# Optimization experiments

Hardware: AMD Instinct MI355X
Metric: run time of the kernel (lower is better)

## Reference

```python
import jax, jax.numpy as jnp
import numpy as np

B, S, H, NH = 32, 512, 768, 12
EC, EU = 4, 4
CAP = 1.0
DH = H // NH
CAPACITY = int(CAP * B / EC)  # Switch-style capacity per common expert


def setup_inputs() -> dict:
    key = jax.random.key(0)
    ks = jax.random.split(key, 10)
    s = 0.02
    E = EC + EU  # experts stacked: [0:EC]=common, [EC:]=unique
    return {
        "hidden_states": jax.random.normal(ks[0], (B, S, H), jnp.float32),
        "attention_mask": jnp.zeros((B, S), jnp.float32),  # additive mask
        "Wq": jax.random.normal(ks[1], (E, H, H), jnp.float32) * s,
        "bq": jnp.zeros((E, H), jnp.float32),
        "Wk": jax.random.normal(ks[2], (E, H, H), jnp.float32) * s,
        "bk": jnp.zeros((E, H), jnp.float32),
        "Wv": jax.random.normal(ks[3], (E, H, H), jnp.float32) * s,
        "bv": jnp.zeros((E, H), jnp.float32),
        "Wo": jax.random.normal(ks[4], (E, H, H), jnp.float32) * s,
        "bo": jnp.zeros((E, H), jnp.float32),
        "Wsc": jax.random.normal(ks[5], (H, EC), jnp.float32) * s,
        "bsc": jnp.zeros((EC,), jnp.float32),
        "Wsu": jax.random.normal(ks[6], (H, EU), jnp.float32) * s,
        "bsu": jnp.zeros((EU,), jnp.float32),
    }


def reference(hidden_states, attention_mask, Wq, bq, Wk, bk, Wv, bv, Wo, bo,
              Wsc, bsc, Wsu, bsu):
    # ---- common routing (per-sequence top-1 over mean-pooled tokens) ----
    h_mean = hidden_states.mean(axis=1)                       # [B,H]
    pc = jax.nn.softmax(h_mean @ Wsc + bsc, axis=-1)          # [B,EC]
    rc = jnp.argmax(pc, axis=-1)                              # [B]
    pc_max = jnp.max(pc, axis=-1)                             # [B]
    # capacity drop: within each expert keep the CAPACITY highest-prob seqs
    order = jnp.argsort(-pc_max)                              # global desc sort
    oh = jax.nn.one_hot(rc[order], EC, dtype=jnp.int32)       # [B,EC]
    rank = jnp.take_along_axis(jnp.cumsum(oh, axis=0), rc[order][:, None], 1)[:, 0]
    kept = jnp.zeros((B,), bool).at[order].set(rank <= CAPACITY)

    # ---- unique routing for dropped sequences (mean is per-sequence, so
    #      computing on the full batch and masking matches torch) ----
    pu = jax.nn.softmax(h_mean @ Wsu + bsu, axis=-1)          # [B,EU]
    ru = jnp.argmax(pu, axis=-1)
    pu_max = jnp.max(pu, axis=-1)

    # per-sequence expert index into stacked [EC+EU] expert params
    eidx = jnp.where(kept, rc, EC + ru)                       # [B]
    # scaling factor p/stop_grad(p): ==1 in fwd, routes grads to the gate
    scale = jnp.where(kept,
                      pc_max / jax.lax.stop_gradient(pc_max),
                      pu_max / jax.lax.stop_gradient(pu_max))

    # ---- gather-dispatch: per-sequence expert weights ----
    Wq_b, Wk_b, Wv_b, Wo_b = Wq[eidx], Wk[eidx], Wv[eidx], Wo[eidx]  # [B,H,H]
    bq_b, bk_b, bv_b, bo_b = bq[eidx], bk[eidx], bv[eidx], bo[eidx]  # [B,H]

    def heads(t):  # [B,S,H] -> [B,NH,S,DH]
        return t.reshape(B, S, NH, DH).transpose(0, 2, 1, 3)

    q = heads(jnp.einsum('bsh,bhd->bsd', hidden_states, Wq_b) + bq_b[:, None, :])
    k = heads(jnp.einsum('bsh,bhd->bsd', hidden_states, Wk_b) + bk_b[:, None, :])
    v = heads(jnp.einsum('bsh,bhd->bsd', hidden_states, Wv_b) + bv_b[:, None, :])

    scores = jnp.einsum('bhsd,bhtd->bhst', q, k) / np.float32(np.sqrt(DH))
    scores = scores + attention_mask[:, None, None, :]        # additive mask
    attn = jax.nn.softmax(scores, axis=-1)
    ctx = jnp.einsum('bhst,bhtd->bhsd', attn, v)
    ctx = ctx.transpose(0, 2, 1, 3).reshape(B, S, H)

    out = jnp.einsum('bsh,bhd->bsd', ctx, Wo_b) + bo_b[:, None, :]
    return out * scale[:, None, None]
```

## Files before the change

kernel.cpp:

```cpp
#include <hip/hip_runtime.h>
#include <hip/hip_bf16.h>

#define B_ 32
#define S_ 512
#define H_ 768
#define NH_ 12
#define DH_ 64
#define EC_ 4
#define CAPN_ 8

using short8  = __attribute__((ext_vector_type(8))) short;
using floatx4 = __attribute__((ext_vector_type(4))) float;
using bf16 = __hip_bfloat16;

__device__ __forceinline__ void gl_lds16(const void* g, void* l) {
  __builtin_amdgcn_global_load_lds(
      (const __attribute__((address_space(1))) unsigned int*)g,
      (__attribute__((address_space(3))) unsigned int*)l, 16, 0, 0);
}

__global__ void k_mean_convert(const float* __restrict__ X, bf16* __restrict__ Xh,
                               float* __restrict__ partial) {
  int idx = blockIdx.x * 256 + threadIdx.x;
  int b = idx / H_, h = idx - b * H_;
  int s0 = blockIdx.y * 64;
  size_t base = ((size_t)b * S_ + s0) * H_ + h;
  float sum = 0.f;
#pragma unroll 8
  for (int s = 0; s < 64; ++s) {
    float v = X[base + (size_t)s * H_];
    Xh[base + (size_t)s * H_] = __float2bfloat16(v);
    sum += v;
  }
  partial[(size_t)blockIdx.y * (B_ * H_) + idx] = sum;
}

__global__ void k_mean_reduce(const float* __restrict__ partial, float* __restrict__ hmean) {
  int idx = blockIdx.x * 256 + threadIdx.x;
  float s = 0.f;
#pragma unroll
  for (int c = 0; c < 8; ++c) s += partial[(size_t)c * (B_ * H_) + idx];
  hmean[idx] = s * (1.f / 512.f);
}

__global__ void k_wt(const float* __restrict__ Wq, const float* __restrict__ Wk,
                     const float* __restrict__ Wv, const float* __restrict__ Wo,
                     bf16* __restrict__ Wt) {
  __shared__ float tile[32][33];
  int z = blockIdx.z;
  const float* Wbase = (z < 8 ? Wq : z < 16 ? Wk : z < 24 ? Wv : Wo) + (size_t)(z & 7) * H_ * H_;
  int k0 = blockIdx.x * 32, n0 = blockIdx.y * 32;
  int tj = threadIdx.x & 31, ti = threadIdx.x >> 5;
#pragma unroll
  for (int r = 0; r < 4; ++r)
    tile[ti + r * 8][tj] = Wbase[(size_t)(k0 + ti + r * 8) * H_ + n0 + tj];
  __syncthreads();
  bf16* out = Wt + (size_t)z * H_ * H_;
#pragma unroll
  for (int r = 0; r < 4; ++r)
    out[(size_t)(n0 + ti + r * 8) * H_ + k0 + tj] = __float2bfloat16(tile[tj][ti + r * 8]);
}

__global__ void k_route(const float* __restrict__ hmean,
                        const float* __restrict__ Wsc, const float* __restrict__ bsc,
                        const float* __restrict__ Wsu, const float* __restrict__ bsu,
                        int* __restrict__ eidx) {
  __shared__ float logit[B_][8];
  __shared__ float pcmax[B_];
  __shared__ int rc_s[B_], ru_s[B_];
  int t = threadIdx.x;
  {
    int b = t >> 3, g = t & 7;
    const float* w = (g < 4) ? (Wsc + g) : (Wsu + (g - 4));
    float acc = (g < 4) ? bsc[g] : bsu[g - 4];
    const float* hm = hmean + (size_t)b * H_;
    for (int hh = 0; hh < H_; ++hh) acc += hm[hh] * w[hh * 4];
    logit[b][g] = acc;
  }
  __syncthreads();
  if (t < B_) {
    float m = logit[t][0]; int a = 0;
    for (int e = 1; e < 4; ++e) if (logit[t][e] > m) { m = logit[t][e]; a = e; }
    float s = 0.f;
    for (int e = 0; e < 4; ++e) s += expf(logit[t][e] - m);
    pcmax[t] = 1.f / s;
    rc_s[t] = a;
    float mu = logit[t][4]; int au = 0;
    for (int e = 1; e < 4; ++e) if (logit[t][4 + e] > mu) { mu = logit[t][4 + e]; au = e; }
    ru_s[t] = au;
  }
  __syncthreads();
  if (t == 0) {
    bool used[B_], kept[B_];
    int cnt[EC_] = {0, 0, 0, 0};
    for (int i = 0; i < B_; ++i) used[i] = false;
    for (int i = 0; i < B_; ++i) {
      int best = 0; float bv = -1e30f;
      for (int j = 0; j < B_; ++j)
        if (!used[j] && pcmax[j] > bv) { bv = pcmax[j]; best = j; }
      used[best] = true;
      kept[best] = (++cnt[rc_s[best]] <= CAPN_);
    }
    for (int i = 0; i < B_; ++i)
      eidx[i] = kept[i] ? rc_s[i] : EC_ + ru_s[i];
  }
}

template <int OMODE>
__global__ __launch_bounds__(256) void k_gemm(
    const bf16* __restrict__ A, const bf16* __restrict__ Wt,
    const float* __restrict__ bias0, const float* __restrict__ bias1,
    const float* __restrict__ bias2,
    void* out0, void* out1, void* out2,
    const int* __restrict__ eidx, int mat0) {
  __shared__ __align__(16) char lds[32768];
  int bz = blockIdx.z;
  int b = blockIdx.y;
  int e = eidx[b];
  int mtile = blockIdx.x & 3, ntile = blockIdx.x >> 2;
  int m0 = mtile * 128, n0 = ntile * 128;
  const bf16* Ab = A + (size_t)b * S_ * H_;
  const bf16* Wb = Wt + (size_t)((mat0 + bz) * 8 + e) * H_ * H_;
  const float* bias = ((bz == 0) ? bias0 : (bz == 1) ? bias1 : bias2) + (size_t)e * H_;
  void* outp = (bz == 0) ? out0 : (bz == 1) ? out1 : out2;

  int t = threadIdx.x, lane = t & 63, w = t >> 6;
  int wm = (w & 1) * 64, wn = (w >> 1) * 64;
  int lm = lane & 15, lq = lane >> 4;

  floatx4 acc[4][4] = {};
  for (int kt = 0; kt < 12; ++kt) {
    __syncthreads();
#pragma unroll
    for (int r = 0; r < 8; ++r) {
      int c = t + r * 256;
      const bf16* g;
      if (c < 1024) {
        int mm = c >> 3, pos = c & 7, kc = pos ^ (mm & 7);
        g = Ab + (size_t)(m0 + mm) * H_ + kt * 64 + kc * 8;
      } else {
        int c2 = c - 1024;
        int nn = c2 >> 3, pos = c2 & 7, kc = pos ^ (nn & 7);
        g = Wb + (size_t)(n0 + nn) * H_ + kt * 64 + kc * 8;
      }
      gl_lds16(g, lds + (size_t)c * 16);
    }
    __syncthreads();
#pragma unroll
    for (int kf = 0; kf < 2; ++kf) {
      int kc = kf * 4 + lq;
      short8 af[4], bf[4];
#pragma unroll
      for (int mf = 0; mf < 4; ++mf) {
        int mm = wm + mf * 16 + lm;
        af[mf] = *(const short8*)(lds + ((size_t)(mm * 8 + (kc ^ (mm & 7)))) * 16);
      }
#pragma unroll
      for (int nf = 0; nf < 4; ++nf) {
        int nn = wn + nf * 16 + lm;
        bf[nf] = *(const short8*)(lds + 16384 + ((size_t)(nn * 8 + (kc ^ (nn & 7)))) * 16);
      }
#pragma unroll
      for (int mf = 0; mf < 4; ++mf)
#pragma unroll
        for (int nf = 0; nf < 4; ++nf)
          acc[mf][nf] = __builtin_amdgcn_mfma_f32_16x16x32_bf16(af[mf], bf[nf], acc[mf][nf], 0, 0, 0);
    }
  }
#pragma unroll
  for (int mf = 0; mf < 4; ++mf) {
#pragma unroll
    for (int nf = 0; nf < 4; ++nf) {
      int n = n0 + wn + nf * 16 + lm;
      float bv = bias[n];
      int mrow = m0 + wm + mf * 16 + lq * 4;
      size_t rowbase = ((size_t)b * S_ + mrow) * H_ + n;
#pragma unroll
      for (int r = 0; r < 4; ++r) {
        float v = acc[mf][nf][r] + bv;
        if (OMODE == 0) ((bf16*)outp)[rowbase + (size_t)r * H_] = __float2bfloat16(v);
        else            ((float*)outp)[rowbase + (size_t)r * H_] = v;
      }
    }
  }
}

__global__ void k_vt(const bf16* __restrict__ V, bf16* __restrict__ Vt) {
  __shared__ __align__(16) unsigned short tile[64][72];
  int sb = blockIdx.x, h = blockIdx.y, b = blockIdx.z;
  int t = threadIdx.x;
  const unsigned short* src =
      (const unsigned short*)V + ((size_t)(b * S_ + sb * 64)) * H_ + h * DH_;
#pragma unroll
  for (int r = 0; r < 2; ++r) {
    int i = (t >> 3) + r * 32, j8 = t & 7;
    uint4 val = *(const uint4*)(src + (size_t)i * H_ + j8 * 8);
    *(uint4*)&tile[i][j8 * 8] = val;
  }
  __syncthreads();
  unsigned short* dst =
      (unsigned short*)Vt + ((size_t)((b * NH_ + h) * 64 + sb * 8)) * 512;
#pragma unroll
  for (int r = 0; r < 2; ++r) {
    int c = t + r * 256;
    int scl = c >> 6, dh = c & 63;
    union { unsigned short u[8]; uint4 v4; } pk;
#pragma unroll
    for (int j = 0; j < 8; ++j) pk.u[j] = tile[scl * 8 + j][dh];
    *(uint4*)(dst + (size_t)c * 8) = pk.v4;
  }
}

__global__ __launch_bounds__(256) void k_attn(
    const bf16* __restrict__ Q, const bf16* __restrict__ K,
    const bf16* __restrict__ Vt, const float* __restrict__ mask,
    bf16* __restrict__ Ctx) {
  __shared__ __align__(16) char ldsQ[4096];
  __shared__ __align__(16) char ldsK[8192];
  __shared__ __align__(16) bf16 sc[32 * 520];
  __shared__ float inv_sum[32];

  int qt = blockIdx.x, h = blockIdx.y, b = blockIdx.z;
  int q0 = qt * 32;
  int t = threadIdx.x, lane = t & 63, w = t >> 6;
  int lm = lane & 15, lq = lane >> 4;

  {
    int s = t >> 3, pos = t & 7, kc = pos ^ (s & 7);
    const bf16* g = Q + ((size_t)(b * S_ + q0 + s)) * H_ + h * DH_ + kc * 8;
    gl_lds16(g, ldsQ + (size_t)t * 16);
  }
  __syncthreads();

  short8 qf[2][2];
#pragma unroll
  for (int mf = 0; mf < 2; ++mf)
#pragma unroll
    for (int kf = 0; kf < 2; ++kf) {
      int srow = mf * 16 + lm, kc = kf * 4 + lq;
      qf[mf][kf] = *(const short8*)(ldsQ + ((size_t)(srow * 8 + (kc ^ (srow & 7)))) * 16);
    }

  for (int kt = 0; kt < 8; ++kt) {
#pragma unroll
    for (int r = 0; r < 2; ++r) {
      int c = t + r * 256;
      int s = c >> 3, pos = c & 7, kc = pos ^ (s & 7);
      const bf16* g = K + ((size_t)(b * S_ + kt * 64 + s)) * H_ + h * DH_ + kc * 8;
      gl_lds16(g, ldsK + (size_t)c * 16);
    }
    __syncthreads();
    floatx4 a2[2] = {};
#pragma unroll
    for (int kf = 0; kf < 2; ++kf) {
      int row = w * 16 + lm, kc = kf * 4 + lq;
      short8 bfr = *(const short8*)(ldsK + ((size_t)(row * 8 + (kc ^ (row & 7)))) * 16);
#pragma unroll
      for (int mf = 0; mf < 2; ++mf)
        a2[mf] = __builtin_amdgcn_mfma_f32_16x16x32_bf16(qf[mf][kf], bfr, a2[mf], 0, 0, 0);
    }
    int col = kt * 64 + w * 16 + lm;
    float mv = mask[(size_t)b * S_ + col];
#pragma unroll
    for (int mf = 0; mf < 2; ++mf)
#pragma unroll
      for (int r = 0; r < 4; ++r) {
        int row = mf * 16 + lq * 4 + r;
        sc[row * 520 + col] = __float2bfloat16(a2[mf][r] * 0.125f + mv);
      }
    __syncthreads();
  }

  {
    int row = t >> 3, seg = t & 7;
    bf16* rp = sc + row * 520;
    float rm = -1e30f;
#pragma unroll 8
    for (int i = 0; i < 64; ++i) rm = fmaxf(rm, __bfloat162float(rp[seg + i * 8]));
    rm = fmaxf(rm, __shfl_xor(rm, 1));
    rm = fmaxf(rm, __shfl_xor(rm, 2));
    rm = fmaxf(rm, __shfl_xor(rm, 4));
    float sum = 0.f;
#pragma unroll 8
    for (int i = 0; i < 64; ++i) {
      float e = __expf(__bfloat162float(rp[seg + i * 8]) - rm);
      sum += e;
      rp[seg + i * 8] = __float2bfloat16(e);
    }
    sum += __shfl_xor(sum, 1);
    sum += __shfl_xor(sum, 2);
    sum += __shfl_xor(sum, 4);
    if (seg == 0) inv_sum[row] = 1.f / sum;
  }
  __syncthreads();

  floatx4 oacc[2] = {};
  const bf16* vbase = Vt + ((size_t)(b * NH_ + h)) * 64 * 512;
  for (int kt = 0; kt < 8; ++kt) {
#pragma unroll
    for (int r = 0; r < 2; ++r) {
      int c = t + r * 256;
      gl_lds16(vbase + ((size_t)(kt * 512 + c)) * 8, ldsK + (size_t)c * 16);
    }
    __syncthreads();
#pragma unroll
    for (int kf = 0; kf < 2; ++kf) {
      int dh = w * 16 + lm;
      short8 bfr = *(const short8*)(ldsK + ((size_t)((kf * 4 + lq) * 64 + dh)) * 16);
#pragma unroll
      for (int mf = 0; mf < 2; ++mf) {
        int row = mf * 16 + lm;
        short8 af = *(const short8*)((const char*)sc +
                        ((size_t)(row * 520 + kt * 64 + kf * 32 + lq * 8)) * 2);
        oacc[mf] = __builtin_amdgcn_mfma_f32_16x16x32_bf16(af, bfr, oacc[mf], 0, 0, 0);
      }
    }
    __syncthreads();
  }
  int dh = w * 16 + lm;
#pragma unroll
  for (int mf = 0; mf < 2; ++mf)
#pragma unroll
    for (int r = 0; r < 4; ++r) {
      int row = mf * 16 + lq * 4 + r;
      float v = oacc[mf][r] * inv_sum[row];
      Ctx[((size_t)(b * S_ + q0 + row)) * H_ + h * DH_ + dh] = __float2bfloat16(v);
    }
}

extern "C" void kernel_launch(void* const* d_in, const int* in_sizes, int n_in,
                              void* d_out, int out_size, void* d_ws, size_t ws_size,
                              hipStream_t stream) {
  const float* X    = (const float*)d_in[0];
  const float* mask = (const float*)d_in[1];
  const float* Wq   = (const float*)d_in[2];
  const float* bq   = (const float*)d_in[3];
  const float* Wk   = (const float*)d_in[4];
  const float* bk   = (const float*)d_in[5];
  const float* Wv   = (const float*)d_in[6];
  const float* bv   = (const float*)d_in[7];
  const float* Wo   = (const float*)d_in[8];
  const float* bo   = (const float*)d_in[9];
  const float* Wsc  = (const float*)d_in[10];
  const float* bsc  = (const float*)d_in[11];
  const float* Wsu  = (const float*)d_in[12];
  const float* bsu  = (const float*)d_in[13];

  char* ws = (char*)d_ws;
  int*   eidx    = (int*)ws;
  float* partial = (float*)(ws + 256);
  float* hmean   = (float*)(ws + 786688);
  bf16*  Xh      = (bf16*)(ws + 884992);
  bf16*  Wt      = (bf16*)(ws + 26050816);
  bf16*  qb      = (bf16*)(ws + 63799552);
  bf16*  kb      = (bf16*)(ws + 88965376);
  bf16*  vb      = (bf16*)(ws + 114131200);
  bf16*  Vt      = (bf16*)(ws + 139297024);
  bf16*  ctx     = Xh;

  k_mean_convert<<<dim3(96, 8), 256, 0, stream>>>(X, Xh, partial);
  k_mean_reduce<<<96, 256, 0, stream>>>(partial, hmean);
  k_wt<<<dim3(24, 24, 32), 256, 0, stream>>>(Wq, Wk, Wv, Wo, Wt);
  k_route<<<1, 256, 0, stream>>>(hmean, Wsc, bsc, Wsu, bsu, eidx);
  k_gemm<0><<<dim3(24, 32, 3), 256, 0, stream>>>(Xh, Wt, bq, bk, bv,
                                                 (void*)qb, (void*)kb, (void*)vb, eidx, 0);
  k_vt<<<dim3(8, NH_, B_), 256, 0, stream>>>(vb, Vt);
  k_attn<<<dim3(16, NH_, B_), 256, 0, stream>>>(qb, kb, Vt, mask, ctx);
  k_gemm<1><<<dim3(24, 32, 1), 256, 0, stream>>>(ctx, Wt, bo, bo, bo,
                                                 d_out, d_out, d_out, eidx, 3);
}
```

Measured before the change: 538.6 us.

## Fuse V transpose into QKV GEMM epilogue and register-resident softmax with double-buffered attention

```diff
diff --git a/kernel.cpp b/kernel.cpp
--- a/kernel.cpp
+++ b/kernel.cpp
@@ -178,135 +178,179 @@
 #pragma unroll
       for (int r = 0; r < 4; ++r) {
         float v = acc[mf][nf][r] + bv;
-        if (OMODE == 0) ((bf16*)outp)[rowbase + (size_t)r * H_] = __float2bfloat16(v);
-        else            ((float*)outp)[rowbase + (size_t)r * H_] = v;
-      }
-    }
-  }
-}
-
-__global__ void k_vt(const bf16* __restrict__ V, bf16* __restrict__ Vt) {
-  __shared__ __align__(16) unsigned short tile[64][72];
-  int sb = blockIdx.x, h = blockIdx.y, b = blockIdx.z;
-  int t = threadIdx.x;
-  const unsigned short* src =
-      (const unsigned short*)V + ((size_t)(b * S_ + sb * 64)) * H_ + h * DH_;
-#pragma unroll
-  for (int r = 0; r < 2; ++r) {
-    int i = (t >> 3) + r * 32, j8 = t & 7;
-    uint4 val = *(const uint4*)(src + (size_t)i * H_ + j8 * 8);
-    *(uint4*)&tile[i][j8 * 8] = val;
-  }
-  __syncthreads();
-  unsigned short* dst =
-      (unsigned short*)Vt + ((size_t)((b * NH_ + h) * 64 + sb * 8)) * 512;
-#pragma unroll
-  for (int r = 0; r < 2; ++r) {
-    int c = t + r * 256;
-    int scl = c >> 6, dh = c & 63;
-    union { unsigned short u[8]; uint4 v4; } pk;
-#pragma unroll
-    for (int j = 0; j < 8; ++j) pk.u[j] = tile[scl * 8 + j][dh];
-    *(uint4*)(dst + (size_t)c * 8) = pk.v4;
-  }
-}
-
-__global__ __launch_bounds__(256) void k_attn(
+        if (OMODE == 0) {
+          if (bz == 2) {
+            int s = mrow + r;
+            ((bf16*)outp)[((size_t)(b * NH_ + (n >> 6))) * 32768 +
+                          (size_t)(s >> 3) * 512 + (n & 63) * 8 + (s & 7)] =
+                __float2bfloat16(v);
+          } else {
+            ((bf16*)outp)[rowbase + (size_t)r * H_] = __float2bfloat16(v);
+          }
+        } else {
+          ((float*)outp)[rowbase + (size_t)r * H_] = v;
+        }
+      }
+    }
+  }
+}
+
+__global__ __launch_bounds__(256, 3) void k_attn(
     const bf16* __restrict__ Q, const bf16* __restrict__ K,
     const bf16* __restrict__ Vt, const float* __restrict__ mask,
     bf16* __restrict__ Ctx) {
-  __shared__ __align__(16) char ldsQ[4096];
-  __shared__ __align__(16) char ldsK[8192];
+  __shared__ __align__(16) char bufA[8192];
+  __shared__ __align__(16) char bufB[8192];
   __shared__ __align__(16) bf16 sc[32 * 520];
-  __shared__ float inv_sum[32];
+  __shared__ float redmax[4][32];
+  __shared__ float redsum[4][32];
 
   int qt = blockIdx.x, h = blockIdx.y, b = blockIdx.z;
   int q0 = qt * 32;
   int t = threadIdx.x, lane = t & 63, w = t >> 6;
   int lm = lane & 15, lq = lane >> 4;
 
+  short8 qf[2][2];
+#pragma unroll
+  for (int mf = 0; mf < 2; ++mf)
+#pragma unroll
+    for (int kf = 0; kf < 2; ++kf)
+      qf[mf][kf] = *(const short8*)(Q + ((size_t)(b * S_ + q0 + mf * 16 + lm)) * H_ +
+                                    h * DH_ + kf * 32 + lq * 8);
+  float mv[8];
+#pragma unroll
+  for (int kt = 0; kt < 8; ++kt)
+    mv[kt] = mask[(size_t)b * S_ + kt * 64 + w * 16 + lm];
+
   {
-    int s = t >> 3, pos = t & 7, kc = pos ^ (s & 7);
-    const bf16* g = Q + ((size_t)(b * S_ + q0 + s)) * H_ + h * DH_ + kc * 8;
-    gl_lds16(g, ldsQ + (size_t)t * 16);
-  }
-  __syncthreads();
-
-  short8 qf[2][2];
-#pragma unroll
-  for (int mf = 0; mf < 2; ++mf)
+#pragma unroll
+    for (int r = 0; r < 2; ++r) {
+      int c = t + r * 256, s = c >> 3, pos = c & 7, kc = pos ^ (s & 7);
+      gl_lds16(K + ((size_t)(b * S_ + s)) * H_ + h * DH_ + kc * 8, bufA + (size_t)c * 16);
+    }
+  }
+  floatx4 acc[8][2] = {};
+  for (int kt = 0; kt < 8; ++kt) {
+    __syncthreads();
+    if (kt < 7) {
+      char* nb = ((kt + 1) & 1) ? bufB : bufA;
+#pragma unroll
+      for (int r = 0; r < 2; ++r) {
+        int c = t + r * 256, s = c >> 3, pos = c & 7, kc = pos ^ (s & 7);
+        gl_lds16(K + ((size_t)(b * S_ + (kt + 1) * 64 + s)) * H_ + h * DH_ + kc * 8,
+                 nb + (size_t)c * 16);
+      }
+    }
+    const char* kb = (kt & 1) ? bufB : bufA;
 #pragma unroll
     for (int kf = 0; kf < 2; ++kf) {
-      int srow = mf * 16 + lm, kc = kf * 4 + lq;
-      qf[mf][kf] = *(const short8*)(ldsQ + ((size_t)(srow * 8 + (kc ^ (srow & 7)))) * 16);
-    }
-
-  for (int kt = 0; kt < 8; ++kt) {
+      int row = w * 16 + lm, kc = kf * 4 + lq;
+      short8 bfr = *(const short8*)(kb + ((size_t)(row * 8 + (kc ^ (row & 7)))) * 16);
+#pragma unroll
+      for (int mf = 0; mf < 2; ++mf)
+        acc[kt][mf] = __builtin_amdgcn_mfma_f32_16x16x32_bf16(qf[mf][kf], bfr, acc[kt][mf], 0, 0, 0);
+    }
+  }
+  __syncthreads();
+
+  const bf16* vbase = Vt + ((size_t)(b * NH_ + h)) * 64 * 512;
+  {
 #pragma unroll
     for (int r = 0; r < 2; ++r) {
       int c = t + r * 256;
-      int s = c >> 3, pos = c & 7, kc = pos ^ (s & 7);
-      const bf16* g = K + ((size_t)(b * S_ + kt * 64 + s)) * H_ + h * DH_ + kc * 8;
-      gl_lds16(g, ldsK + (size_t)c * 16);
-    }
-    __syncthreads();
-    floatx4 a2[2] = {};
-#pragma unroll
-    for (int kf = 0; kf < 2; ++kf) {
-      int row = w * 16 + lm, kc = kf * 4 + lq;
-      short8 bfr = *(const short8*)(ldsK + ((size_t)(row * 8 + (kc ^ (row & 7)))) * 16);
-#pragma unroll
-      for (int mf = 0; mf < 2; ++mf)
-        a2[mf] = __builtin_amdgcn_mfma_f32_16x16x32_bf16(qf[mf][kf], bfr, a2[mf], 0, 0, 0);
-    }
+      gl_lds16(vbase + (size_t)c * 8, bufA + (size_t)c * 16);
+    }
+  }
+
+  float rmax[2][4];
+#pragma unroll
+  for (int mf = 0; mf < 2; ++mf)
+#pragma unroll
+    for (int r = 0; r < 4; ++r) rmax[mf][r] = -1e30f;
+#pragma unroll
+  for (int kt = 0; kt < 8; ++kt)
+#pragma unroll
+    for (int mf = 0; mf < 2; ++mf)
+#pragma unroll
+      for (int r = 0; r < 4; ++r) {
+        float s = acc[kt][mf][r] * 0.125f + mv[kt];
+        acc[kt][mf][r] = s;
+        rmax[mf][r] = fmaxf(rmax[mf][r], s);
+      }
+#pragma unroll
+  for (int st = 1; st < 16; st <<= 1)
+#pragma unroll
+    for (int mf = 0; mf < 2; ++mf)
+#pragma unroll
+      for (int r = 0; r < 4; ++r)
+        rmax[mf][r] = fmaxf(rmax[mf][r], __shfl_xor(rmax[mf][r], st, 64));
+  if (lm == 0) {
+#pragma unroll
+    for (int mf = 0; mf < 2; ++mf)
+#pragma unroll
+      for (int r = 0; r < 4; ++r) redmax[w][mf * 16 + lq * 4 + r] = rmax[mf][r];
+  }
+  __syncthreads();
+#pragma unroll
+  for (int mf = 0; mf < 2; ++mf)
+#pragma unroll
+    for (int r = 0; r < 4; ++r) {
+      int row = mf * 16 + lq * 4 + r;
+      rmax[mf][r] = fmaxf(fmaxf(redmax[0][row], redmax[1][row]),
+                          fmaxf(redmax[2][row], redmax[3][row]));
+    }
+  float rsum[2][4] = {};
+#pragma unroll
+  for (int kt = 0; kt < 8; ++kt) {
     int col = kt * 64 + w * 16 + lm;
-    float mv = mask[(size_t)b * S_ + col];
 #pragma unroll
     for (int mf = 0; mf < 2; ++mf)
 #pragma unroll
       for (int r = 0; r < 4; ++r) {
-        int row = mf * 16 + lq * 4 + r;
-        sc[row * 520 + col] = __float2bfloat16(a2[mf][r] * 0.125f + mv);
-      }
-    __syncthreads();
-  }
-
-  {
-    int row = t >> 3, seg = t & 7;
-    bf16* rp = sc + row * 520;
-    float rm = -1e30f;
-#pragma unroll 8
-    for (int i = 0; i < 64; ++i) rm = fmaxf(rm, __bfloat162float(rp[seg + i * 8]));
-    rm = fmaxf(rm, __shfl_xor(rm, 1));
-    rm = fmaxf(rm, __shfl_xor(rm, 2));
-    rm = fmaxf(rm, __shfl_xor(rm, 4));
-    float sum = 0.f;
-#pragma unroll 8
-    for (int i = 0; i < 64; ++i) {
-      float e = __expf(__bfloat162float(rp[seg + i * 8]) - rm);
-      sum += e;
-      rp[seg + i * 8] = __float2bfloat16(e);
-    }
-    sum += __shfl_xor(sum, 1);
-    sum += __shfl_xor(sum, 2);
-    sum += __shfl_xor(sum, 4);
-    if (seg == 0) inv_sum[row] = 1.f / sum;
-  }
-  __syncthreads();
+        float e = __expf(acc[kt][mf][r] - rmax[mf][r]);
+        rsum[mf][r] += e;
+        sc[(mf * 16 + lq * 4 + r) * 520 + col] = __float2bfloat16(e);
+      }
+  }
+#pragma unroll
+  for (int st = 1; st < 16; st <<= 1)
+#pragma unroll
+    for (int mf = 0; mf < 2; ++mf)
+#pragma unroll
+      for (int r = 0; r < 4; ++r)
+        rsum[mf][r] += __shfl_xor(rsum[mf][r], st, 64);
+  if (lm == 0) {
+#pragma unroll
+    for (int mf = 0; mf < 2; ++mf)
+#pragma unroll
+      for (int r = 0; r < 4; ++r) redsum[w][mf * 16 + lq * 4 + r] = rsum[mf][r];
+  }
+  __syncthreads();
+  float inv[2][4];
+#pragma unroll
+  for (int mf = 0; mf < 2; ++mf)
+#pragma unroll
+    for (int r = 0; r < 4; ++r) {
+      int row = mf * 16 + lq * 4 + r;
+      inv[mf][r] = 1.f / (redsum[0][row] + redsum[1][row] + redsum[2][row] + redsum[3][row]);
+    }
 
   floatx4 oacc[2] = {};
-  const bf16* vbase = Vt + ((size_t)(b * NH_ + h)) * 64 * 512;
   for (int kt = 0; kt < 8; ++kt) {
-#pragma unroll
-    for (int r = 0; r < 2; ++r) {
-      int c = t + r * 256;
-      gl_lds16(vbase + ((size_t)(kt * 512 + c)) * 8, ldsK + (size_t)c * 16);
-    }
-    __syncthreads();
+    if (kt) __syncthreads();
+    if (kt < 7) {
+      char* nb = ((kt + 1) & 1) ? bufB : bufA;
+#pragma unroll
+      for (int r = 0; r < 2; ++r) {
+        int c = t + r * 256;
+        gl_lds16(vbase + ((size_t)((kt + 1) * 512 + c)) * 8, nb + (size_t)c * 16);
+      }
+    }
+    const char* vb = (kt & 1) ? bufB : bufA;
 #pragma unroll
     for (int kf = 0; kf < 2; ++kf) {
       int dh = w * 16 + lm;
-      short8 bfr = *(const short8*)(ldsK + ((size_t)((kf * 4 + lq) * 64 + dh)) * 16);
+      short8 bfr = *(const short8*)(vb + ((size_t)((kf * 4 + lq) * 64 + dh)) * 16);
 #pragma unroll
       for (int mf = 0; mf < 2; ++mf) {
         int row = mf * 16 + lm;
@@ -315,7 +359,6 @@
         oacc[mf] = __builtin_amdgcn_mfma_f32_16x16x32_bf16(af, bfr, oacc[mf], 0, 0, 0);
       }
     }
-    __syncthreads();
   }
   int dh = w * 16 + lm;
 #pragma unroll
@@ -323,8 +366,8 @@
 #pragma unroll
     for (int r = 0; r < 4; ++r) {
       int row = mf * 16 + lq * 4 + r;
-      float v = oacc[mf][r] * inv_sum[row];
-      Ctx[((size_t)(b * S_ + q0 + row)) * H_ + h * DH_ + dh] = __float2bfloat16(v);
+      Ctx[((size_t)(b * S_ + q0 + row)) * H_ + h * DH_ + dh] =
+          __float2bfloat16(oacc[mf][r] * inv[mf][r]);
     }
 }
 
@@ -354,7 +397,6 @@
   bf16*  Wt      = (bf16*)(ws + 26050816);
   bf16*  qb      = (bf16*)(ws + 63799552);
   bf16*  kb      = (bf16*)(ws + 88965376);
-  bf16*  vb      = (bf16*)(ws + 114131200);
   bf16*  Vt      = (bf16*)(ws + 139297024);
   bf16*  ctx     = Xh;
 
@@ -363,8 +405,7 @@
   k_wt<<<dim3(24, 24, 32), 256, 0, stream>>>(Wq, Wk, Wv, Wo, Wt);
   k_route<<<1, 256, 0, stream>>>(hmean, Wsc, bsc, Wsu, bsu, eidx);
   k_gemm<0><<<dim3(24, 32, 3), 256, 0, stream>>>(Xh, Wt, bq, bk, bv,
-                                                 (void*)qb, (void*)kb, (void*)vb, eidx, 0);
-  k_vt<<<dim3(8, NH_, B_), 256, 0, stream>>>(vb, Vt);
+                                                 (void*)qb, (void*)kb, (void*)Vt, eidx, 0);
   k_attn<<<dim3(16, NH_, B_), 256, 0, stream>>>(qb, kb, Vt, mask, ctx);
   k_gemm<1><<<dim3(24, 32, 1), 256, 0, stream>>>(ctx, Wt, bo, bo, bo,
                                                  d_out, d_out, d_out, eidx, 3);
```

After: 498.7 us. 1.08x faster.
